# Kernel tuning notes

Hardware: AMD Instinct MI355X
Metric: run time of the kernel (lower is better)

The kernel has to match this reference:

```python
import jax, jax.numpy as jnp
import numpy as np

N_TOK, D_MODEL, N_EXPERTS, TOP_K = 8192, 512, 8, 2


def setup_inputs() -> dict:
    key = jax.random.key(0)
    k1, k2, k3 = jax.random.split(key, 3)
    x = jax.random.normal(k1, (N_TOK, D_MODEL), jnp.float32)
    w_gate = jax.random.normal(k2, (D_MODEL, N_EXPERTS), jnp.float32) * 0.02
    expert_w = jax.random.normal(k3, (N_EXPERTS, D_MODEL, D_MODEL), jnp.float32) * (D_MODEL ** -0.5)
    return {"x": x, "w_gate": w_gate, "expert_w": expert_w, "top_k": TOP_K}


def _cv_sq(v):
    m = jnp.mean(v)
    return jnp.var(v) / (m * m + 1e-10)


def reference(x, w_gate, expert_w, top_k):
    # ---- Gate (clean top-k gating, eval mode of noisy-top-k) ----
    logits = x @ w_gate                              # [N, E]
    top_vals, top_idx = jax.lax.top_k(logits, top_k)  # [N, k]
    top_gates = jax.nn.softmax(top_vals, axis=-1)
    n, e = logits.shape
    gates = jnp.zeros((n, e), x.dtype).at[jnp.arange(n)[:, None], top_idx].set(top_gates)

    # ---- dispatch -> per-expert GEMM -> log-domain combine ----
    # combine(): stitched = cat(expert_out).exp() * nonzero_gates; index_add over
    # batch index; zeros -> eps; log. Dense-equivalent (tokens with gate 0
    # contribute exactly nothing):
    expert_out = jnp.einsum('nd,edf->nef', x, expert_w)   # per-expert outputs [N, E, D]
    combined = jnp.einsum('ne,nef->nf', gates, jnp.exp(expert_out))  # [N, D]
    eps = np.float32(np.finfo(np.float64).eps)
    combined = jnp.where(combined == 0, eps, combined)
    out = jnp.log(combined)

    # ---- load-balance aux loss: cv^2(importance) + cv^2(load) ----
    importance = gates.sum(0)
    load = (gates > 0).sum(0).astype(x.dtype)
    balance_loss = _cv_sq(importance) + _cv_sq(load)
    return out, balance_loss
```

## Files before the change

kernel.cpp:

```cpp
#include <hip/hip_runtime.h>
#include <hip/hip_bf16.h>
#include <math.h>

#define N_TOK 8192
#define D 512
#define NE 8

typedef float f32x4 __attribute__((ext_vector_type(4)));
typedef __bf16 bf16x8 __attribute__((ext_vector_type(8)));
typedef unsigned short u16;
typedef u16 u16x8 __attribute__((ext_vector_type(8)));

#define OFF_TOKE  256
#define OFF_TOKG  65792
#define OFF_BUCK  131328
#define OFF_XB    (1u << 20)
#define OFF_EWT   (OFF_XB + 8u * 1024 * 1024)
#define OFF_Y     (OFF_EWT + 4u * 1024 * 1024)

__device__ __forceinline__ u16 f2b(float v) {
    __hip_bfloat16 h = __float2bfloat16(v);
    return *reinterpret_cast<u16*>(&h);
}
__device__ __forceinline__ float b2f(u16 u) {
    __hip_bfloat16 h;
    *reinterpret_cast<u16*>(&h) = u;
    return __bfloat162float(h);
}

typedef __attribute__((address_space(1))) const void* gp1_t;
typedef __attribute__((address_space(3))) void* lp3_t;
__device__ __forceinline__ void gload16(const void* g, void* l) {
    __builtin_amdgcn_global_load_lds((gp1_t)g, (lp3_t)l, 16, 0, 0);
}

__global__ __launch_bounds__(256) void gate_prep_kernel(
    const float* __restrict__ x, const float* __restrict__ wg,
    const float* __restrict__ ew,
    int* __restrict__ tok_e, float* __restrict__ tok_g, u16* __restrict__ xb,
    u16* __restrict__ ewt)
{
    __shared__ __align__(16) float sbuf[64 * 65];
    int b = blockIdx.x;
    int tid = threadIdx.x;

    if (b >= 2048) {
        int pb = b - 2048;
        float (*tile)[65] = (float(*)[65])sbuf;
        int e = pb >> 6, dt = (pb >> 3) & 7, ftl = pb & 7;
        int c = tid & 63, rq = tid >> 6;
        const float* src = ew + (size_t)e * D * D + (size_t)(dt * 64) * D + ftl * 64;
#pragma unroll
        for (int i = 0; i < 16; ++i) {
            int r = i * 4 + rq;
            tile[r][c] = src[(size_t)r * D + c];
        }
        __syncthreads();
        u16* dst = ewt + (size_t)e * D * D + (size_t)(ftl * 64) * D + dt * 64;
#pragma unroll
        for (int i = 0; i < 16; ++i) {
            int f = i * 4 + rq;
            dst[(size_t)f * D + c] = f2b(tile[c][f]);
        }
        return;
    }

    float* wgs = sbuf;
    for (int i = tid; i < NE * D; i += 256) {
        int d = i >> 3, e = i & 7;
        wgs[e * D + d] = wg[i];
    }
    __syncthreads();

    int wave = tid >> 6, lane = tid & 63;
    int n = b * 4 + wave;
    const float* xr = x + (size_t)n * D;
    u16* xbr = xb + (size_t)n * D;

    float p[NE];
#pragma unroll
    for (int e = 0; e < NE; ++e) p[e] = 0.f;
#pragma unroll
    for (int it = 0; it < 8; ++it) {
        float xv = xr[it * 64 + lane];
        xbr[it * 64 + lane] = f2b(xv);
#pragma unroll
        for (int e = 0; e < NE; ++e)
            p[e] += xv * wgs[e * D + it * 64 + lane];
    }
#pragma unroll
    for (int off = 32; off > 0; off >>= 1) {
#pragma unroll
        for (int e = 0; e < NE; ++e)
            p[e] += __shfl_xor(p[e], off);
    }

    if (lane == 0) {
        int e1 = 0; float v1 = p[0];
#pragma unroll
        for (int e = 1; e < NE; ++e) if (p[e] > v1) { v1 = p[e]; e1 = e; }
        int e2 = -1; float v2 = -INFINITY;
#pragma unroll
        for (int e = 0; e < NE; ++e) if (e != e1 && p[e] > v2) { v2 = p[e]; e2 = e; }
        float t = __expf(v2 - v1);
        float inv = 1.f / (1.f + t);
        tok_e[2 * n] = e1;     tok_e[2 * n + 1] = e2;
        tok_g[2 * n] = inv;    tok_g[2 * n + 1] = t * inv;
    }
}

__global__ __launch_bounds__(256) void bucketize_kernel(
    const int* __restrict__ tok_e, const float* __restrict__ tok_g,
    int* __restrict__ count, float* __restrict__ imp, int* __restrict__ bucket)
{
    __shared__ int lcnt[NE], lbase[NE];
    __shared__ float limp[NE];
    int tid = threadIdx.x;
    if (tid < NE) { lcnt[tid] = 0; limp[tid] = 0.f; }
    __syncthreads();

    int n = blockIdx.x * 256 + tid;
    int e1 = tok_e[2 * n], e2 = tok_e[2 * n + 1];
    float g1 = tok_g[2 * n], g2 = tok_g[2 * n + 1];
    int o1 = atomicAdd(&lcnt[e1], 1);
    int o2 = atomicAdd(&lcnt[e2], 1);
    atomicAdd(&limp[e1], g1);
    atomicAdd(&limp[e2], g2);
    __syncthreads();
    if (tid < NE) {
        lbase[tid] = atomicAdd(&count[tid], lcnt[tid]);
        atomicAdd(&imp[tid], limp[tid]);
    }
    __syncthreads();
    bucket[e1 * N_TOK + lbase[e1] + o1] = 2 * n;
    bucket[e2 * N_TOK + lbase[e2] + o2] = 2 * n + 1;
}

__global__ __launch_bounds__(256) void moe_gemm(
    const u16* __restrict__ xb, const u16* __restrict__ ewt,
    const int* __restrict__ count, const int* __restrict__ bucket,
    u16* __restrict__ y)
{
    int b = blockIdx.x;
    int ft = b & 3;
    int tt = (b >> 2) & 63;
    int e  = b >> 8;
    int cnt = count[e];
    if (tt * 128 >= cnt) return;

    __shared__ int sl[128];
    __shared__ __align__(16) u16 smem[16384];
    u16* As = smem;
    u16* Bs = smem + 8192;

    int tid = threadIdx.x;
    if (tid < 128) {
        int idx = tt * 128 + tid;
        sl[tid] = (idx < cnt) ? bucket[e * N_TOK + idx] : -1;
    }
    __syncthreads();

    int w = tid >> 6, l = tid & 63;
    int c8 = (l & 3) * 8;
    int r0 = w * 32 + (l >> 2);
    int r1 = r0 + 16;
    int s0 = sl[r0], s1 = sl[r1];
    int ta0 = (s0 < 0) ? 0 : (s0 >> 1);
    int ta1 = (s1 < 0) ? 0 : (s1 >> 1);
    const u16* gA0 = xb + (size_t)ta0 * D + c8;
    const u16* gA1 = xb + (size_t)ta1 * D + c8;
    const u16* gB0 = ewt + ((size_t)e * D + ft * 128 + r0) * D + c8;
    const u16* gB1 = ewt + ((size_t)e * D + ft * 128 + r1) * D + c8;
    u16* lA0 = &As[(w * 32) * 32];
    u16* lA1 = &As[(w * 32 + 16) * 32];
    u16* lB0 = &Bs[(w * 32) * 32];
    u16* lB1 = &Bs[(w * 32 + 16) * 32];

    int wm = w & 1, wn = w >> 1;
    int lm = l & 15, quad = l >> 4, kq = quad * 8;

    f32x4 acc[4][4] = {};

    for (int kc = 0; kc < 16; ++kc) {
        __syncthreads();
        gload16(gA0 + kc * 32, lA0);
        gload16(gA1 + kc * 32, lA1);
        gload16(gB0 + kc * 32, lB0);
        gload16(gB1 + kc * 32, lB1);
        __syncthreads();

        bf16x8 af[4], bfv[4];
#pragma unroll
        for (int i = 0; i < 4; ++i)
            af[i] = *(const bf16x8*)&As[(wm * 64 + i * 16 + lm) * 32 + kq];
#pragma unroll
        for (int j = 0; j < 4; ++j)
            bfv[j] = *(const bf16x8*)&Bs[(wn * 64 + j * 16 + lm) * 32 + kq];
#pragma unroll
        for (int i = 0; i < 4; ++i)
#pragma unroll
            for (int j = 0; j < 4; ++j)
                acc[i][j] = __builtin_amdgcn_mfma_f32_16x16x32_bf16(
                    af[i], bfv[j], acc[i][j], 0, 0, 0);
    }

    __syncthreads();
    u16* Es = smem + w * 2304;
#pragma unroll
    for (int h = 0; h < 2; ++h) {
#pragma unroll
        for (int i2 = 0; i2 < 2; ++i2) {
            int i = h * 2 + i2;
#pragma unroll
            for (int j = 0; j < 4; ++j)
#pragma unroll
                for (int r = 0; r < 4; ++r)
                    Es[(i2 * 16 + quad * 4 + r) * 72 + j * 16 + lm] =
                        f2b(acc[i][j][r]);
        }
        int row = l >> 1, hc = l & 1;
        int s = sl[wm * 64 + h * 32 + row];
        const u16* src = Es + row * 72 + hc * 32;
        u16* dst = y + (size_t)((s < 0) ? 0 : s) * D + ft * 128 + wn * 64 + hc * 32;
        if (s >= 0) {
#pragma unroll
            for (int c = 0; c < 4; ++c)
                *(u16x8*)(dst + c * 8) = *(const u16x8*)(src + c * 8);
        }
    }
}

__global__ __launch_bounds__(256) void combine_kernel(
    const u16* __restrict__ y, const float* __restrict__ tok_g,
    const int* __restrict__ count, const float* __restrict__ imp,
    float* __restrict__ out)
{
    if (blockIdx.x == 4096) {
        if (threadIdx.x == 0) {
            float mi = 0.f, ml = 0.f;
            for (int e = 0; e < NE; ++e) { mi += imp[e]; ml += (float)count[e]; }
            mi *= 0.125f; ml *= 0.125f;
            float vi = 0.f, vl = 0.f;
            for (int e = 0; e < NE; ++e) {
                float di = imp[e] - mi;          vi += di * di;
                float dl = (float)count[e] - ml; vl += dl * dl;
            }
            vi *= 0.125f; vl *= 0.125f;
            out[N_TOK * D] = vi / (mi * mi + 1e-10f) + vl / (ml * ml + 1e-10f);
        }
        return;
    }
    int idx = blockIdx.x * 256 + threadIdx.x;
    int n = idx >> 7;
    int c = (idx & 127) * 4;
    const ushort4 ua = *(const ushort4*)(y + (size_t)(2 * n) * D + c);
    const ushort4 ub = *(const ushort4*)(y + (size_t)(2 * n + 1) * D + c);
    float g1 = tok_g[2 * n], g2 = tok_g[2 * n + 1];
    const float eps = 2.2204460492503131e-16f;
    float4 r;
    float v;
    v = g1 * __expf(b2f(ua.x)) + g2 * __expf(b2f(ub.x)); r.x = __logf(v == 0.f ? eps : v);
    v = g1 * __expf(b2f(ua.y)) + g2 * __expf(b2f(ub.y)); r.y = __logf(v == 0.f ? eps : v);
    v = g1 * __expf(b2f(ua.z)) + g2 * __expf(b2f(ub.z)); r.z = __logf(v == 0.f ? eps : v);
    v = g1 * __expf(b2f(ua.w)) + g2 * __expf(b2f(ub.w)); r.w = __logf(v == 0.f ? eps : v);
    *(float4*)(out + (size_t)n * D + c) = r;
}

extern "C" void kernel_launch(void* const* d_in, const int* in_sizes, int n_in,
                              void* d_out, int out_size, void* d_ws, size_t ws_size,
                              hipStream_t stream)
{
    const float* x  = (const float*)d_in[0];
    const float* wg = (const float*)d_in[1];
    const float* ew = (const float*)d_in[2];
    char* ws = (char*)d_ws;
    int*   count  = (int*)(ws + 0);
    float* imp    = (float*)(ws + 64);
    int*   tok_e  = (int*)(ws + OFF_TOKE);
    float* tok_g  = (float*)(ws + OFF_TOKG);
    int*   bucket = (int*)(ws + OFF_BUCK);
    u16*   xb     = (u16*)(ws + OFF_XB);
    u16*   ewt    = (u16*)(ws + OFF_EWT);
    u16*   y      = (u16*)(ws + OFF_Y);
    float* out    = (float*)d_out;

    hipMemsetAsync(ws, 0, 128, stream);
    gate_prep_kernel<<<2048 + 512, 256, 0, stream>>>(x, wg, ew, tok_e, tok_g, xb, ewt);
    bucketize_kernel<<<N_TOK / 256, 256, 0, stream>>>(tok_e, tok_g, count, imp, bucket);
    moe_gemm<<<NE * 64 * 4, 256, 0, stream>>>(xb, ewt, count, bucket, y);
    combine_kernel<<<4097, 256, 0, stream>>>(y, tok_g, count, imp, out);
}
```

Measured before the change: 120.9 us.

## Double-buffer LDS tiles in MoE GEMM to overlap global loads with MFMA

Splits the 32KB shared buffer into two 16KB stages (A and B tiles of 4096 elements each) and prefetches the next K-chunk via direct-to-LDS loads while the current chunk is consumed. Explicit vmcnt waits and raw s_barrier calls replace the two __syncthreads per iteration. The aim is to hide global memory latency behind MFMA work. A barrier is also added in the epilogue loop, since the reused shared region now spans the whole buffer.

```diff
diff --git a/kernel.cpp b/kernel.cpp
--- a/kernel.cpp
+++ b/kernel.cpp
@@ -150,8 +150,6 @@
 
     __shared__ int sl[128];
     __shared__ __align__(16) u16 smem[16384];
-    u16* As = smem;
-    u16* Bs = smem + 8192;
 
     int tid = threadIdx.x;
     if (tid < 128) {
@@ -171,24 +169,35 @@
     const u16* gA1 = xb + (size_t)ta1 * D + c8;
     const u16* gB0 = ewt + ((size_t)e * D + ft * 128 + r0) * D + c8;
     const u16* gB1 = ewt + ((size_t)e * D + ft * 128 + r1) * D + c8;
-    u16* lA0 = &As[(w * 32) * 32];
-    u16* lA1 = &As[(w * 32 + 16) * 32];
-    u16* lB0 = &Bs[(w * 32) * 32];
-    u16* lB1 = &Bs[(w * 32 + 16) * 32];
 
     int wm = w & 1, wn = w >> 1;
     int lm = l & 15, quad = l >> 4, kq = quad * 8;
 
     f32x4 acc[4][4] = {};
 
+    auto stage = [&](int p, int kc) {
+        u16* As = smem + p * 8192;
+        u16* Bs = As + 4096;
+        gload16(gA0 + kc * 32, &As[(w * 32) * 32]);
+        gload16(gA1 + kc * 32, &As[(w * 32 + 16) * 32]);
+        gload16(gB0 + kc * 32, &Bs[(w * 32) * 32]);
+        gload16(gB1 + kc * 32, &Bs[(w * 32 + 16) * 32]);
+    };
+
+    stage(0, 0);
+    int cur = 0;
     for (int kc = 0; kc < 16; ++kc) {
-        __syncthreads();
-        gload16(gA0 + kc * 32, lA0);
-        gload16(gA1 + kc * 32, lA1);
-        gload16(gB0 + kc * 32, lB0);
-        gload16(gB1 + kc * 32, lB1);
-        __syncthreads();
-
+        if (kc < 15) {
+            stage(cur ^ 1, kc + 1);
+            asm volatile("s_waitcnt vmcnt(4)" ::: "memory");
+        } else {
+            asm volatile("s_waitcnt vmcnt(0)" ::: "memory");
+        }
+        __builtin_amdgcn_s_barrier();
+        asm volatile("" ::: "memory");
+
+        const u16* As = smem + cur * 8192;
+        const u16* Bs = As + 4096;
         bf16x8 af[4], bfv[4];
 #pragma unroll
         for (int i = 0; i < 4; ++i)
@@ -202,6 +211,10 @@
             for (int j = 0; j < 4; ++j)
                 acc[i][j] = __builtin_amdgcn_mfma_f32_16x16x32_bf16(
                     af[i], bfv[j], acc[i][j], 0, 0, 0);
+
+        asm volatile("s_waitcnt lgkmcnt(0)" ::: "memory");
+        __builtin_amdgcn_s_barrier();
+        cur ^= 1;
     }
 
     __syncthreads();
@@ -227,6 +240,7 @@
             for (int c = 0; c < 4; ++c)
                 *(u16x8*)(dst + c * 8) = *(const u16x8*)(src + c * 8);
         }
+        __syncthreads();
     }
 }
 
```

Measured after the change: 123.7 us. 1.02x slower.
